# Performance work log

Hardware: AMD Instinct MI355X
Metric: run time of the kernel (lower is better)

The kernel has to match this reference:

```python
import jax, jax.numpy as jnp
import numpy as np

D_MODEL = 1024
D_SAE = 16384
BATCH = 4096
EPS = 1e-8

def _layer_norm(v):
    # v: [B, D]; matches torch branch with keepdim=True
    mean = v.mean(axis=1, keepdims=True)
    var = ((v - mean) ** 2).mean(axis=1, keepdims=True)
    return (v - mean) / jnp.sqrt(var + EPS)

def setup_inputs() -> dict:
    key = jax.random.key(0)
    k1, k2 = jax.random.split(key)
    x = jax.random.normal(k1, (BATCH, 2 * D_MODEL), dtype=jnp.float32)
    # kaiming_uniform on [d_model, d_sae]: bound = sqrt(6 / fan_in), fan_in = d_sae (torch default mode='fan_in' on dim 1)
    bound = float(np.sqrt(6.0 / D_SAE))
    W_enc = jax.random.uniform(k2, (D_MODEL, D_SAE), dtype=jnp.float32, minval=-bound, maxval=bound)
    W_dec = W_enc.T  # init ties decoder to encoder transpose
    b_enc = jnp.zeros((D_SAE,), dtype=jnp.float32)
    b_dec = jnp.zeros((D_MODEL,), dtype=jnp.float32)
    return {"x": x, "W_enc": W_enc, "b_enc": b_enc, "W_dec": W_dec, "b_dec": b_dec, "k": 64}

def reference(x, W_enc, b_enc, W_dec, b_dec, k):
    B = x.shape[0]
    d_model = W_enc.shape[0]
    src = x[:, :d_model]
    tgt = x[:, d_model:]
    # standardize_method == 'layer_norm_and_diff_layer_norm'
    diff = _layer_norm(_layer_norm(tgt) - _layer_norm(src))  # [B, D]
    # encode
    acts = jax.nn.relu(diff @ W_enc + b_enc)  # [B, F]
    # batch top-k on decoder-norm-scaled scores
    dec_norms = jnp.linalg.norm(W_dec, axis=1)  # [F]
    flat_scores = (acts * dec_norms).reshape(-1)  # [B*F]
    _, topk_idx = jax.lax.top_k(flat_scores, k * B)
    mask = jnp.zeros_like(flat_scores).at[topk_idx].set(1.0).reshape(B, -1)
    sparse_acts = acts * mask  # [B, F]
    # decode
    recon = sparse_acts @ W_dec + b_dec  # [B, D]
    return recon
```

## Files before the change

kernel.cpp:

```cpp
#include <hip/hip_runtime.h>
#include <math.h>

#define D_MODEL 1024
#define D_SAE   16384
#define BATCH   4096
#define NTOT    (1ull * BATCH * D_SAE)
#define LN_EPS  1e-8
#define EPS_M   3e-4f
#define ROW_CAP 256
#define CAND_CAP  (4 * 1024 * 1024)
#define CAND2_CAP 65536

using bf16x8 = __attribute__((ext_vector_type(8))) short;
using f32x4  = __attribute__((ext_vector_type(4))) float;

__device__ inline unsigned short f2bf(float f) {
  unsigned u = __float_as_uint(f);
  return (unsigned short)((u + 0x7fffu + ((u >> 16) & 1u)) >> 16);
}
__device__ inline float bf2f(unsigned short h) {
  return __uint_as_float((unsigned)h << 16);
}

__device__ inline double blockReduceSum256(double v, double* lds) {
#pragma unroll
  for (int off = 32; off > 0; off >>= 1) v += __shfl_down(v, off, 64);
  int lane = threadIdx.x & 63, wid = threadIdx.x >> 6;
  __syncthreads();
  if (lane == 0) lds[wid] = v;
  __syncthreads();
  return lds[0] + lds[1] + lds[2] + lds[3];
}
__device__ inline int blockReduceSumInt256(int v, int* lds) {
#pragma unroll
  for (int off = 32; off > 0; off >>= 1) v += __shfl_down(v, off, 64);
  int lane = threadIdx.x & 63, wid = threadIdx.x >> 6;
  __syncthreads();
  if (lane == 0) lds[wid] = v;
  __syncthreads();
  return lds[0] + lds[1] + lds[2] + lds[3];
}

__device__ inline int wave_append(bool pred, int* counter) {
  unsigned long long m = __ballot(pred);
  int lane = threadIdx.x & 63;
  int pos = -1;
  if (m) {
    int ldr = __ffsll((long long)m) - 1;
    int base = 0;
    if (lane == ldr) base = atomicAdd(counter, __popcll(m));
    base = __shfl(base, ldr, 64);
    if (pred) pos = base + __popcll(m & ((1ull << lane) - 1ull));
  }
  return pos;
}

__device__ inline void hist_scan_desc(const int* __restrict__ hist, int nbins, int need,
                                      int& bsel, int& cumsel) {
  int t = threadIdx.x;
  int chunk = nbins >> 6;
  int topbase = nbins - t * chunk;
  int psum = 0;
  for (int i = 1; i <= chunk; ++i) psum += hist[topbase - i];
  int incl = psum;
#pragma unroll
  for (int off = 1; off < 64; off <<= 1) {
    int v = __shfl_up(incl, off, 64);
    if (t >= off) incl += v;
  }
  int excl = incl - psum;
  bool hit = (excl < need) && (excl + psum >= need);
  unsigned long long m = __ballot(hit);
  int tb = m ? (__ffsll((long long)m) - 1) : 63;
  int exb = __shfl(excl, tb, 64);
  int res_b = 0, res_c = 0;
  if (t == tb) {
    int c = exb;
    int b = nbins - tb * chunk - 1;
    int bend = b - chunk;
    for (; b > 0 && b > bend; --b) {
      int cc = hist[b];
      if (c + cc >= need) break;
      c += cc;
    }
    res_b = b; res_c = c;
  }
  bsel = __shfl(res_b, tb, 64);
  cumsel = __shfl(res_c, tb, 64);
}

__device__ inline void ln_row_fp64(const float* __restrict__ row, double* lds, double d[4]) {
  int t = threadIdx.x;
  float4 s4 = *(const float4*)(row + t * 4);
  float4 t4 = *(const float4*)(row + D_MODEL + t * 4);
  double s[4] = {s4.x, s4.y, s4.z, s4.w};
  double tt[4] = {t4.x, t4.y, t4.z, t4.w};
  double ms = blockReduceSum256(s[0] + s[1] + s[2] + s[3], lds) / D_MODEL;
  double mt = blockReduceSum256(tt[0] + tt[1] + tt[2] + tt[3], lds) / D_MODEL;
  double vs = 0, vt = 0;
#pragma unroll
  for (int i = 0; i < 4; i++) { double a = s[i] - ms; vs += a * a; a = tt[i] - mt; vt += a * a; }
  vs = blockReduceSum256(vs, lds) / D_MODEL;
  vt = blockReduceSum256(vt, lds) / D_MODEL;
  double rs = sqrt(vs + LN_EPS), rt = sqrt(vt + LN_EPS);
  double u[4];
#pragma unroll
  for (int i = 0; i < 4; i++) u[i] = (tt[i] - mt) / rt - (s[i] - ms) / rs;
  double mu = blockReduceSum256(u[0] + u[1] + u[2] + u[3], lds) / D_MODEL;
  double vu = 0;
#pragma unroll
  for (int i = 0; i < 4; i++) { double a = u[i] - mu; vu += a * a; }
  vu = blockReduceSum256(vu, lds) / D_MODEL;
  double ru = sqrt(vu + LN_EPS);
#pragma unroll
  for (int i = 0; i < 4; i++) d[i] = (u[i] - mu) / ru;
}

__global__ __launch_bounds__(256) void ln_kernel(const float* __restrict__ x,
                                                 short* __restrict__ Ahi, short* __restrict__ Alo) {
  int wv = threadIdx.x >> 6, lane = threadIdx.x & 63;
  int b = (blockIdx.x << 2) | wv;
  const float* row = x + (size_t)b * (2 * D_MODEL);
  float s[16], t[16];
  const float4* s4p = (const float4*)(row + lane * 16);
  const float4* t4p = (const float4*)(row + D_MODEL + lane * 16);
  double sum_s = 0, sum_t = 0;
#pragma unroll
  for (int q = 0; q < 4; ++q) {
    float4 a = s4p[q], c = t4p[q];
    s[q * 4 + 0] = a.x; s[q * 4 + 1] = a.y; s[q * 4 + 2] = a.z; s[q * 4 + 3] = a.w;
    t[q * 4 + 0] = c.x; t[q * 4 + 1] = c.y; t[q * 4 + 2] = c.z; t[q * 4 + 3] = c.w;
  }
#pragma unroll
  for (int i = 0; i < 16; ++i) { sum_s += s[i]; sum_t += t[i]; }
#pragma unroll
  for (int off = 1; off < 64; off <<= 1) {
    sum_s += __shfl_xor(sum_s, off, 64);
    sum_t += __shfl_xor(sum_t, off, 64);
  }
  double ms = sum_s / D_MODEL, mt_ = sum_t / D_MODEL;
  double vs = 0, vt = 0;
#pragma unroll
  for (int i = 0; i < 16; ++i) {
    double a = s[i] - ms; vs += a * a;
    double c = t[i] - mt_; vt += c * c;
  }
#pragma unroll
  for (int off = 1; off < 64; off <<= 1) {
    vs += __shfl_xor(vs, off, 64);
    vt += __shfl_xor(vt, off, 64);
  }
  double rs = sqrt(vs / D_MODEL + LN_EPS), rt = sqrt(vt / D_MODEL + LN_EPS);
  double u[16], su = 0;
#pragma unroll
  for (int i = 0; i < 16; ++i) { u[i] = (t[i] - mt_) / rt - (s[i] - ms) / rs; su += u[i]; }
#pragma unroll
  for (int off = 1; off < 64; off <<= 1) su += __shfl_xor(su, off, 64);
  double mu = su / D_MODEL, vu = 0;
#pragma unroll
  for (int i = 0; i < 16; ++i) { double a = u[i] - mu; vu += a * a; }
#pragma unroll
  for (int off = 1; off < 64; off <<= 1) vu += __shfl_xor(vu, off, 64);
  double ru = sqrt(vu / D_MODEL + LN_EPS);
  int mtb = b >> 7, ml = b & 127;
#pragma unroll
  for (int blk8 = 0; blk8 < 2; ++blk8) {
    short h8[8], l8[8];
#pragma unroll
    for (int e = 0; e < 8; ++e) {
      int i = blk8 * 8 + e;
      double dd = (u[i] - mu) / ru;
      float f = (float)dd;
      unsigned short hh = f2bf(f);
      h8[e] = (short)hh;
      l8[e] = (short)f2bf(f - bf2f(hh));
    }
    int gi = lane * 16 + blk8 * 8;
    int ks = gi >> 5, kc = (gi >> 3) & 3;
    size_t base = ((((size_t)mtb * 32 + ks) * 4 + kc) * 128 + ml) * 8;
    *(float4*)&Ahi[base] = *(float4*)h8;
    *(float4*)&Alo[base] = *(float4*)l8;
  }
}

__global__ __launch_bounds__(256) void norm_kernel(const float* __restrict__ Wdec,
                                                   double* __restrict__ g64, float* __restrict__ g32) {
  int wv = threadIdx.x >> 6, lane = threadIdx.x & 63;
  int j = (blockIdx.x << 2) | wv;
  const float4* rowp = (const float4*)(Wdec + (size_t)j * D_MODEL);
  double a = 0;
#pragma unroll
  for (int q = 0; q < 4; ++q) {
    float4 w = rowp[lane + q * 64];
    a += (double)w.x * w.x + (double)w.y * w.y + (double)w.z * w.z + (double)w.w * w.w;
  }
#pragma unroll
  for (int off = 32; off > 0; off >>= 1) a += __shfl_down(a, off, 64);
  if (lane == 0) { double g = sqrt(a); g64[j] = g; g32[j] = (float)g; }
}

__global__ __launch_bounds__(256) void wsplit_kernel(const float* __restrict__ Wenc,
                                                     short* __restrict__ Whi, short* __restrict__ Wlo) {
  __shared__ short sh[4096];
  __shared__ short sl[4096];
  int blk = blockIdx.x;
  int nt = blk >> 5, ks = blk & 31;
  int t = threadIdx.x;
  int r = t >> 3;
  int cg = t & 7;
  int kc = r >> 3, e = r & 7;
  const float* src = Wenc + (size_t)(ks * 32 + r) * D_SAE + nt * 128 + cg;
#pragma unroll
  for (int j = 0; j < 16; ++j) {
    float f = src[j * 8];
    unsigned short hh = f2bf(f);
    short ll = (short)f2bf(f - bf2f(hh));
    int c = j * 8 + cg;
    sh[kc * 1024 + c * 8 + e] = (short)hh;
    sl[kc * 1024 + c * 8 + e] = ll;
  }
  __syncthreads();
  size_t obase = ((size_t)nt * 32 + ks) * 4096;
  *(float4*)&Whi[obase + t * 16]     = *(const float4*)&sh[t * 16];
  *(float4*)&Whi[obase + t * 16 + 8] = *(const float4*)&sh[t * 16 + 8];
  *(float4*)&Wlo[obase + t * 16]     = *(const float4*)&sl[t * 16];
  *(float4*)&Wlo[obase + t * 16 + 8] = *(const float4*)&sl[t * 16 + 8];
}

__global__ __launch_bounds__(256) void wdecsplit_kernel(const float* __restrict__ Wdec,
                                                        short* __restrict__ wdech) {
  int j = blockIdx.x, t = threadIdx.x;
  float4 w = *(const float4*)(Wdec + (size_t)j * D_MODEL + t * 4);
  short4 h;
  h.x = (short)f2bf(w.x); h.y = (short)f2bf(w.y);
  h.z = (short)f2bf(w.z); h.w = (short)f2bf(w.w);
  *(short4*)&wdech[(size_t)j * D_MODEL + t * 4] = h;
}

__global__ __launch_bounds__(256) void hist_gemm(
    const short* __restrict__ Whi, const short* __restrict__ Ahi,
    const float* __restrict__ benc, const float* __restrict__ g32,
    int* __restrict__ ghist) {
  __shared__ short sA[4096];
  __shared__ short sB[4096];
  __shared__ int h[4][2048];
  const int tid = threadIdx.x;
  const int lane = tid & 63;
  const int w = tid >> 6;
  const int wm = (w >> 1) * 64, wn = (w & 1) * 64;
  int lin = blockIdx.x;
  int mt = lin >> 7, nt = lin & 127;
  const int col0 = nt * 128;
  for (int i = tid; i < 8192; i += 256) ((int*)h)[i] = 0;
  const size_t atile = (size_t)mt * 131072;
  const size_t btile = (size_t)nt * 131072;
  f32x4 acc[4][4] = {};
  const int kcl = lane >> 4, l15 = lane & 15;

  float4 a0, a1, b0, b1;
  {
    const float4* ah4 = (const float4*)(Ahi + atile);
    const float4* bh4 = (const float4*)(Whi + btile);
    a0 = ah4[tid]; a1 = ah4[tid + 256];
    b0 = bh4[tid]; b1 = bh4[tid + 256];
  }
  for (int ks = 0; ks < 32; ++ks) {
    __syncthreads();
    *(float4*)&sA[(size_t)tid * 8] = a0;
    *(float4*)&sA[(size_t)(tid + 256) * 8] = a1;
    *(float4*)&sB[(size_t)tid * 8] = b0;
    *(float4*)&sB[(size_t)(tid + 256) * 8] = b1;
    __syncthreads();
    if (ks < 31) {
      const float4* ah4 = (const float4*)(Ahi + atile + (ks + 1) * 4096);
      const float4* bh4 = (const float4*)(Whi + btile + (ks + 1) * 4096);
      a0 = ah4[tid]; a1 = ah4[tid + 256];
      b0 = bh4[tid]; b1 = bh4[tid + 256];
    }
    bf16x8 ahf[4];
#pragma unroll
    for (int fm = 0; fm < 4; ++fm)
      ahf[fm] = *(const bf16x8*)&sA[(kcl * 128 + wm + fm * 16 + l15) * 8];
#pragma unroll
    for (int fn = 0; fn < 4; ++fn) {
      bf16x8 bh = *(const bf16x8*)&sB[(kcl * 128 + wn + fn * 16 + l15) * 8];
#pragma unroll
      for (int fm = 0; fm < 4; ++fm)
        acc[fm][fn] = __builtin_amdgcn_mfma_f32_16x16x32_bf16(ahf[fm], bh, acc[fm][fn], 0, 0, 0);
    }
  }
#pragma unroll
  for (int fn = 0; fn < 4; ++fn) {
    int col = col0 + wn + fn * 16 + l15;
    float g = g32[col], be = benc[col];
#pragma unroll
    for (int fm = 0; fm < 4; ++fm) {
#pragma unroll
      for (int r = 0; r < 4; ++r) {
        float z = acc[fm][fn][r] + be;
        float s = z > 0.f ? z * g : 0.f;
        unsigned bits = __float_as_uint(s);
        if (bits) atomicAdd(&h[w][bits >> 21], 1);
      }
    }
  }
  __syncthreads();
  for (int i = tid; i < 2048; i += 256) {
    int v = h[0][i] + h[1][i] + h[2][i] + h[3][i];
    if (v) atomicAdd(&ghist[i], v);
  }
}

__global__ __launch_bounds__(256, 3) void extract_gemm128(
    const short* __restrict__ Whi, const short* __restrict__ Wlo,
    const short* __restrict__ Ahi, const short* __restrict__ Alo,
    const float* __restrict__ benc, const float* __restrict__ g32,
    int* __restrict__ ctrl, int* __restrict__ cand_idx, float* __restrict__ cand_sc,
    int* __restrict__ ghist) {
  __shared__ short sA[8192];
  __shared__ short sB[8192];

  const int tid = threadIdx.x;
  const int lane = tid & 63;
  const int w = tid >> 6;
  const int wm = (w >> 1) * 64, wn = (w & 1) * 64;

  int lin = blockIdx.x;
  int xcd = lin & 7, j = lin >> 3;
  int mt = (xcd << 2) | (j & 3);
  int nt = j >> 2;
  const int row0 = mt * 128, col0 = nt * 128;

  const size_t atile = (size_t)mt * 131072;
  const size_t btile = (size_t)nt * 131072;

  f32x4 acc[4][4] = {};
  const int kcl = lane >> 4, l15 = lane & 15;

  float4 a0, a1, a2, a3, b0, b1, b2, b3;
  {
    const float4* ah4 = (const float4*)(Ahi + atile);
    const float4* al4 = (const float4*)(Alo + atile);
    const float4* bh4 = (const float4*)(Whi + btile);
    const float4* bl4 = (const float4*)(Wlo + btile);
    a0 = ah4[tid]; a1 = ah4[tid + 256];
    a2 = al4[tid]; a3 = al4[tid + 256];
    b0 = bh4[tid]; b1 = bh4[tid + 256];
    b2 = bl4[tid]; b3 = bl4[tid + 256];
  }

  for (int ks = 0; ks < 32; ++ks) {
    __syncthreads();
    *(float4*)&sA[(size_t)tid * 8] = a0;
    *(float4*)&sA[(size_t)(tid + 256) * 8] = a1;
    *(float4*)&sA[(size_t)(512 + tid) * 8] = a2;
    *(float4*)&sA[(size_t)(512 + tid + 256) * 8] = a3;
    *(float4*)&sB[(size_t)tid * 8] = b0;
    *(float4*)&sB[(size_t)(tid + 256) * 8] = b1;
    *(float4*)&sB[(size_t)(512 + tid) * 8] = b2;
    *(float4*)&sB[(size_t)(512 + tid + 256) * 8] = b3;
    __syncthreads();
    if (ks < 31) {
      const int o = (ks + 1) * 4096;
      const float4* ah4 = (const float4*)(Ahi + atile + o);
      const float4* al4 = (const float4*)(Alo + atile + o);
      const float4* bh4 = (const float4*)(Whi + btile + o);
      const float4* bl4 = (const float4*)(Wlo + btile + o);
      a0 = ah4[tid]; a1 = ah4[tid + 256];
      a2 = al4[tid]; a3 = al4[tid + 256];
      b0 = bh4[tid]; b1 = bh4[tid + 256];
      b2 = bl4[tid]; b3 = bl4[tid + 256];
    }
    bf16x8 ahf[4], alf[4];
#pragma unroll
    for (int fm = 0; fm < 4; ++fm) {
      int off = (kcl * 128 + wm + fm * 16 + l15) * 8;
      ahf[fm] = *(const bf16x8*)&sA[off];
      alf[fm] = *(const bf16x8*)&sA[4096 + off];
    }
#pragma unroll
    for (int fn = 0; fn < 4; ++fn) {
      int boff = (kcl * 128 + wn + fn * 16 + l15) * 8;
      bf16x8 bh = *(const bf16x8*)&sB[boff];
      bf16x8 bl = *(const bf16x8*)&sB[4096 + boff];
#pragma unroll
      for (int fm = 0; fm < 4; ++fm) {
        acc[fm][fn] = __builtin_amdgcn_mfma_f32_16x16x32_bf16(ahf[fm], bh, acc[fm][fn], 0, 0, 0);
        acc[fm][fn] = __builtin_amdgcn_mfma_f32_16x16x32_bf16(alf[fm], bh, acc[fm][fn], 0, 0, 0);
        acc[fm][fn] = __builtin_amdgcn_mfma_f32_16x16x32_bf16(ahf[fm], bl, acc[fm][fn], 0, 0, 0);
      }
    }
  }

  int* hh = (int*)sA;
  const int l4r = lane >> 4;
  unsigned thrBits = (unsigned)ctrl[1];
  __syncthreads();
  for (int i = tid; i < 2050; i += 256) hh[i] = 0;
  __syncthreads();
  int cnt = 0;
#pragma unroll
  for (int fn = 0; fn < 4; ++fn) {
    int col = col0 + wn + fn * 16 + l15;
    float g = g32[col], be = benc[col];
#pragma unroll
    for (int fm = 0; fm < 4; ++fm) {
#pragma unroll
      for (int r = 0; r < 4; ++r) {
        float z = acc[fm][fn][r] + be;
        float s = z > 0.f ? z * g : 0.f;
        unsigned bits = __float_as_uint(s);
        if (bits >= thrBits) { cnt++; atomicAdd(&hh[bits >> 21], 1); }
      }
    }
  }
  int my = 0;
  if (cnt) my = atomicAdd(&hh[2048], cnt);
  __syncthreads();
  if (tid == 0) hh[2049] = atomicAdd(&ctrl[2], hh[2048]);
  for (int i = tid; i < 2048; i += 256)
    if (hh[i]) atomicAdd(&ghist[i], hh[i]);
  __syncthreads();
  int pos = hh[2049] + my;
#pragma unroll
  for (int fn = 0; fn < 4; ++fn) {
    int col = col0 + wn + fn * 16 + l15;
    float g = g32[col], be = benc[col];
#pragma unroll
    for (int fm = 0; fm < 4; ++fm) {
      int rowb = row0 + wm + fm * 16 + l4r * 4;
#pragma unroll
      for (int r = 0; r < 4; ++r) {
        float z = acc[fm][fn][r] + be;
        float s = z > 0.f ? z * g : 0.f;
        if (__float_as_uint(s) >= thrBits) {
          if (pos < CAND_CAP) { cand_idx[pos] = (rowb + r) * D_SAE + col; cand_sc[pos] = s; }
          pos++;
        }
      }
    }
  }
}

template <int MODE>
__global__ __launch_bounds__(256) void mfma_gemm(
    const float* __restrict__ Wenc,
    const short* __restrict__ Ahi, const short* __restrict__ Alo,
    const float* __restrict__ benc, const float* __restrict__ g32,
    int* __restrict__ ghist, int* __restrict__ ctrl,
    int* __restrict__ cand_idx, float* __restrict__ cand_sc) {
  __shared__ short sA[8192];
  __shared__ short sB[8192];
  __shared__ int h[(MODE == 0) ? 2048 : 2];
  const int tid = threadIdx.x;
  const int lane = tid & 63;
  const int w = tid >> 6;
  const int wm = (w >> 1) * 64, wn = (w & 1) * 64;
  int lin = blockIdx.x;
  int mt, nt;
  if (MODE == 0) { mt = lin >> 7; nt = lin & 127; }
  else { int xcd = lin & 7, j = lin >> 3; mt = j & 31; nt = (xcd << 4) | (j >> 5); }
  const int row0 = mt * 128, col0 = nt * 128;
  if (MODE == 0) { for (int i = tid; i < 2048; i += 256) h[i] = 0; }
  else if (tid == 0) h[0] = 0;
  const int nl = tid & 127;
  const int half = tid >> 7;
  const float* wbase = Wenc + (size_t)col0 + nl;
  const size_t atile = (size_t)mt * 131072;
  f32x4 acc[4][4] = {};
  const int kcl = lane >> 4, l15 = lane & 15;
  float4 a0, a1, a2, a3;
  float bfv[16];
  {
    const float4* ah4 = (const float4*)(Ahi + atile);
    const float4* al4 = (const float4*)(Alo + atile);
    a0 = ah4[tid]; a1 = ah4[tid + 256];
    a2 = al4[tid]; a3 = al4[tid + 256];
#pragma unroll
    for (int p = 0; p < 4; ++p)
#pragma unroll
      for (int i = 0; i < 4; ++i)
        bfv[p * 4 + i] = wbase[(size_t)(p * 8 + half * 4 + i) * D_SAE];
  }
  for (int ks = 0; ks < 32; ++ks) {
    short hb[16], lb[16];
#pragma unroll
    for (int q = 0; q < 16; ++q) {
      unsigned short hh = f2bf(bfv[q]);
      hb[q] = (short)hh;
      lb[q] = (short)f2bf(bfv[q] - bf2f(hh));
    }
    __syncthreads();
    *(float4*)&sA[(size_t)tid * 8] = a0;
    *(float4*)&sA[(size_t)(tid + 256) * 8] = a1;
    *(float4*)&sA[(size_t)(512 + tid) * 8] = a2;
    *(float4*)&sA[(size_t)(512 + tid + 256) * 8] = a3;
#pragma unroll
    for (int p = 0; p < 4; ++p) {
      int boff = p * 1024 + nl * 8 + half * 4;
      *(short4*)&sB[boff] = make_short4(hb[p * 4], hb[p * 4 + 1], hb[p * 4 + 2], hb[p * 4 + 3]);
      *(short4*)&sB[4096 + boff] = make_short4(lb[p * 4], lb[p * 4 + 1], lb[p * 4 + 2], lb[p * 4 + 3]);
    }
    __syncthreads();
    if (ks < 31) {
      const float4* ah4 = (const float4*)(Ahi + atile + (ks + 1) * 4096);
      const float4* al4 = (const float4*)(Alo + atile + (ks + 1) * 4096);
      a0 = ah4[tid]; a1 = ah4[tid + 256];
      a2 = al4[tid]; a3 = al4[tid + 256];
      const int k0n = (ks + 1) * 32;
#pragma unroll
      for (int p = 0; p < 4; ++p)
#pragma unroll
        for (int i = 0; i < 4; ++i)
          bfv[p * 4 + i] = wbase[(size_t)(k0n + p * 8 + half * 4 + i) * D_SAE];
    }
    bf16x8 ahf[4], alf[4];
#pragma unroll
    for (int fm = 0; fm < 4; ++fm) {
      int off = (kcl * 128 + wm + fm * 16 + l15) * 8;
      ahf[fm] = *(const bf16x8*)&sA[off];
      alf[fm] = *(const bf16x8*)&sA[4096 + off];
    }
#pragma unroll
    for (int fn = 0; fn < 4; ++fn) {
      int boff = (kcl * 128 + wn + fn * 16 + l15) * 8;
      bf16x8 bh = *(const bf16x8*)&sB[boff];
      bf16x8 bl = *(const bf16x8*)&sB[4096 + boff];
#pragma unroll
      for (int fm = 0; fm < 4; ++fm) {
        acc[fm][fn] = __builtin_amdgcn_mfma_f32_16x16x32_bf16(ahf[fm], bh, acc[fm][fn], 0, 0, 0);
        acc[fm][fn] = __builtin_amdgcn_mfma_f32_16x16x32_bf16(alf[fm], bh, acc[fm][fn], 0, 0, 0);
        acc[fm][fn] = __builtin_amdgcn_mfma_f32_16x16x32_bf16(ahf[fm], bl, acc[fm][fn], 0, 0, 0);
      }
    }
  }
  const int l4r = lane >> 4;
  if (MODE == 0) {
#pragma unroll
    for (int fn = 0; fn < 4; ++fn) {
      int col = col0 + wn + fn * 16 + l15;
      float g = g32[col], be = benc[col];
#pragma unroll
      for (int fm = 0; fm < 4; ++fm) {
#pragma unroll
        for (int r = 0; r < 4; ++r) {
          float z = acc[fm][fn][r] + be;
          float s = z > 0.f ? z * g : 0.f;
          unsigned bits = __float_as_uint(s);
          if (bits) atomicAdd(&h[bits >> 21], 1);
        }
      }
    }
    __syncthreads();
    for (int i = tid; i < 2048; i += 256)
      if (h[i]) atomicAdd(&ghist[i], h[i]);
  } else {
    unsigned thrBits = (unsigned)ctrl[1];
    int cnt = 0;
#pragma unroll
    for (int fn = 0; fn < 4; ++fn) {
      int col = col0 + wn + fn * 16 + l15;
      float g = g32[col], be = benc[col];
#pragma unroll
      for (int fm = 0; fm < 4; ++fm) {
#pragma unroll
        for (int r = 0; r < 4; ++r) {
          float z = acc[fm][fn][r] + be;
          float s = z > 0.f ? z * g : 0.f;
          cnt += (__float_as_uint(s) >= thrBits) ? 1 : 0;
        }
      }
    }
    int my = 0;
    if (cnt) my = atomicAdd(&h[0], cnt);
    __syncthreads();
    if (tid == 0) h[1] = atomicAdd(&ctrl[2], h[0]);
    __syncthreads();
    int pos = h[1] + my;
#pragma unroll
    for (int fn = 0; fn < 4; ++fn) {
      int col = col0 + wn + fn * 16 + l15;
      float g = g32[col], be = benc[col];
#pragma unroll
      for (int fm = 0; fm < 4; ++fm) {
        int rowb = row0 + wm + fm * 16 + l4r * 4;
#pragma unroll
        for (int r = 0; r < 4; ++r) {
          float z = acc[fm][fn][r] + be;
          float s = z > 0.f ? z * g : 0.f;
          if (__float_as_uint(s) >= thrBits) {
            if (pos < CAND_CAP) { cand_idx[pos] = (rowb + r) * D_SAE + col; cand_sc[pos] = s; }
            pos++;
          }
        }
      }
    }
  }
}

__global__ void find_coarse_kernel(const int* __restrict__ gh, int* ctrl,
                                   const int* __restrict__ kptr, int sub) {
  long long kB = (long long)kptr[0] * BATCH;
  long long needl = (kB + 500000 + sub - 1) / sub;
  long long fl = 720000 / sub;
  if (needl < fl) needl = fl;
  int b, cum;
  hist_scan_desc(gh, 2048, (int)needl, b, cum);
  if (threadIdx.x == 0) {
    long long est_incl = (long long)sub * (cum + gh[b]);
    if (est_incl > 3500000LL && (long long)sub * cum >= kB + 120000LL) b = b + 1;
    ctrl[1] = (int)(((unsigned)b) << 21);
  }
}

__global__ __launch_bounds__(256) void chist_kernel(const float* __restrict__ cand_sc,
                                                    const int* __restrict__ ctrl,
                                                    int* __restrict__ ghist, int pass) {
  __shared__ int h[2048];
  int nb = (pass == 2) ? 1024 : 2048;
  for (int i = threadIdx.x; i < nb; i += 256) h[i] = 0;
  __syncthreads();
  int n = ctrl[2]; if (n > CAND_CAP) n = CAND_CAP;
  unsigned sel1 = 0, sel22 = 0;
  if (pass == 1) sel1 = (unsigned)ctrl[3];
  if (pass == 2) sel22 = ((unsigned)ctrl[3] << 11) | (unsigned)ctrl[5];
  for (int i = blockIdx.x * 256 + threadIdx.x; i < n; i += gridDim.x * 256) {
    unsigned bits = __float_as_uint(cand_sc[i]);
    if (pass == 0) atomicAdd(&h[bits >> 21], 1);
    else if (pass == 1) { if ((bits >> 21) == sel1) atomicAdd(&h[(bits >> 10) & 0x7FFu], 1); }
    else { if ((bits >> 10) == sel22) atomicAdd(&h[bits & 0x3FFu], 1); }
  }
  __syncthreads();
  for (int i = threadIdx.x; i < nb; i += 256)
    if (h[i]) atomicAdd(&ghist[i], h[i]);
}

__global__ void cfind_kernel(const int* __restrict__ hist, int* ctrl,
                             const int* __restrict__ kptr, int pass) {
  int kB = kptr[0] * BATCH;
  int need, nbins;
  if (pass == 0)      { need = kB;                       nbins = 2048; }
  else if (pass == 1) { need = kB - ctrl[4];             nbins = 2048; }
  else                { need = kB - ctrl[4] - ctrl[6];   nbins = 1024; }
  int b, cum;
  hist_scan_desc(hist, nbins, need, b, cum);
  if (threadIdx.x == 0) {
    if (pass == 0)      { ctrl[3] = b; ctrl[4] = cum; }
    else if (pass == 1) { ctrl[5] = b; ctrl[6] = cum; }
    else {
      unsigned vbits = ((unsigned)ctrl[3] << 21) | ((unsigned)ctrl[5] << 10) | (unsigned)b;
      float V = __uint_as_float(vbits);
      float* cf = (float*)ctrl;
      cf[8] = V; cf[9] = V + EPS_M; cf[10] = V - EPS_M;
    }
  }
}

__global__ __launch_bounds__(256) void band_kernel(const int* __restrict__ cand_idx,
    const float* __restrict__ cand_sc, const float* __restrict__ g32,
    int* ctrl, int* row_cnt, int* row_feat, float* row_act, int* cand2_idx) {
  const float* cf = (const float*)ctrl;
  float hi = cf[9], lo = cf[10];
  int n = ctrl[2]; if (n > CAND_CAP) n = CAND_CAP;
  int lane = threadIdx.x & 63;
  int defc = 0;
  for (int i = blockIdx.x * 256 + threadIdx.x; i < n; i += gridDim.x * 256) {
    float s = cand_sc[i];
    int flat = cand_idx[i];
    if (s > hi) {
      int b = flat >> 14, j = flat & (D_SAE - 1);
      int p = atomicAdd(&row_cnt[b], 1);
      if (p < ROW_CAP) { row_feat[b * ROW_CAP + p] = j; row_act[b * ROW_CAP + p] = s / g32[j]; }
      defc++;
    }
    bool isc = (s <= hi) && (s >= lo);
    int pos = wave_append(isc, &ctrl[12]);
    if (isc && pos >= 0 && pos < CAND2_CAP) cand2_idx[pos] = flat;
  }
#pragma unroll
  for (int off = 32; off > 0; off >>= 1) defc += __shfl_down(defc, off, 64);
  if (lane == 0 && defc) atomicAdd(&ctrl[11], defc);
}

__global__ __launch_bounds__(256) void cand2_score_kernel(const int* __restrict__ ctrl,
    const int* __restrict__ cand2_idx, const float* __restrict__ x,
    const float* __restrict__ Wdec, const float* __restrict__ benc,
    const double* __restrict__ g64, double* __restrict__ cand2_sc) {
  __shared__ double lds[4];
  int n2 = ctrl[12]; if (n2 > CAND2_CAP) n2 = CAND2_CAP;
  int t = threadIdx.x;
  for (int c = blockIdx.x; c < n2; c += gridDim.x) {
    int flat = cand2_idx[c];
    int b = flat >> 14, j = flat & (D_SAE - 1);
    double d[4];
    ln_row_fp64(x + (size_t)b * (2 * D_MODEL), lds, d);
    float4 w4 = *(const float4*)(Wdec + (size_t)j * D_MODEL + t * 4);
    double a = d[0] * (double)w4.x + d[1] * (double)w4.y + d[2] * (double)w4.z + d[3] * (double)w4.w;
    double z = blockReduceSum256(a, lds) + (double)benc[j];
    double sc = z > 0 ? z * g64[j] : 0.0;
    if (t == 0) cand2_sc[c] = sc;
  }
}

__global__ __launch_bounds__(256) void cand2_rank_kernel(const int* __restrict__ ctrl,
    const int* __restrict__ cand2_idx, const double* __restrict__ cand2_sc,
    const double* __restrict__ g64, const int* __restrict__ kptr,
    int* row_cnt, int* row_feat, float* row_act) {
  __shared__ int lds[4];
  int n2 = ctrl[12]; if (n2 > CAND2_CAP) n2 = CAND2_CAP;
  int kB = kptr[0] * BATCH;
  int fill = kB - ctrl[11];
  int t = threadIdx.x;
  for (int c = blockIdx.x; c < n2; c += gridDim.x) {
    double sc = cand2_sc[c];
    int fc = cand2_idx[c];
    int cnt = 0;
    for (int y = t; y < n2; y += 256) {
      double sy = cand2_sc[y];
      if (sy > sc || (sy == sc && cand2_idx[y] < fc)) cnt++;
    }
    cnt = blockReduceSumInt256(cnt, lds);
    if (t == 0 && cnt < fill) {
      int b = fc >> 14, j = fc & (D_SAE - 1);
      int p = atomicAdd(&row_cnt[b], 1);
      if (p < ROW_CAP) { row_feat[b * ROW_CAP + p] = j; row_act[b * ROW_CAP + p] = (float)(sc / g64[j]); }
    }
  }
}

__global__ __launch_bounds__(256) void recon_bf16_kernel(const int* __restrict__ row_cnt,
    const int* __restrict__ row_feat, const float* __restrict__ row_act,
    const short* __restrict__ wdech, const float* __restrict__ bdec, float* __restrict__ out) {
  int b = blockIdx.x, t = threadIdx.x;
  float4 acc0 = *(const float4*)&bdec[t * 4];
  float4 acc1 = make_float4(0.f, 0.f, 0.f, 0.f);
  int n = row_cnt[b]; if (n > ROW_CAP) n = ROW_CAP;
  const int* rf = row_feat + (size_t)b * ROW_CAP;
  const float* ra = row_act + (size_t)b * ROW_CAP;
  int p = 0;
  for (; p + 2 <= n; p += 2) {
    int j0 = rf[p], j1 = rf[p + 1];
    float v0 = ra[p], v1 = ra[p + 1];
    short4 h0 = *(const short4*)&wdech[(size_t)j0 * D_MODEL + t * 4];
    short4 h1 = *(const short4*)&wdech[(size_t)j1 * D_MODEL + t * 4];
    acc0.x += v0 * bf2f((unsigned short)h0.x); acc0.y += v0 * bf2f((unsigned short)h0.y);
    acc0.z += v0 * bf2f((unsigned short)h0.z); acc0.w += v0 * bf2f((unsigned short)h0.w);
    acc1.x += v1 * bf2f((unsigned short)h1.x); acc1.y += v1 * bf2f((unsigned short)h1.y);
    acc1.z += v1 * bf2f((unsigned short)h1.z); acc1.w += v1 * bf2f((unsigned short)h1.w);
  }
  if (p < n) {
    int j0 = rf[p]; float v0 = ra[p];
    short4 h0 = *(const short4*)&wdech[(size_t)j0 * D_MODEL + t * 4];
    acc0.x += v0 * bf2f((unsigned short)h0.x); acc0.y += v0 * bf2f((unsigned short)h0.y);
    acc0.z += v0 * bf2f((unsigned short)h0.z); acc0.w += v0 * bf2f((unsigned short)h0.w);
  }
  acc0.x += acc1.x; acc0.y += acc1.y; acc0.z += acc1.z; acc0.w += acc1.w;
  *(float4*)(out + (size_t)b * D_MODEL + t * 4) = acc0;
}

__global__ __launch_bounds__(256) void recon_kernel(const int* __restrict__ row_cnt,
    const int* __restrict__ row_feat, const float* __restrict__ row_act,
    const float* __restrict__ Wdec, const float* __restrict__ bdec, float* __restrict__ out) {
  int b = blockIdx.x, t = threadIdx.x;
  float4 acc0 = *(const float4*)&bdec[t * 4];
  float4 acc1 = make_float4(0.f, 0.f, 0.f, 0.f);
  int n = row_cnt[b]; if (n > ROW_CAP) n = ROW_CAP;
  const int* rf = row_feat + (size_t)b * ROW_CAP;
  const float* ra = row_act + (size_t)b * ROW_CAP;
  int p = 0;
  for (; p + 2 <= n; p += 2) {
    int j0 = rf[p], j1 = rf[p + 1];
    float v0 = ra[p], v1 = ra[p + 1];
    float4 w0 = *(const float4*)(Wdec + (size_t)j0 * D_MODEL + t * 4);
    float4 w1 = *(const float4*)(Wdec + (size_t)j1 * D_MODEL + t * 4);
    acc0.x += v0 * w0.x; acc0.y += v0 * w0.y; acc0.z += v0 * w0.z; acc0.w += v0 * w0.w;
    acc1.x += v1 * w1.x; acc1.y += v1 * w1.y; acc1.z += v1 * w1.z; acc1.w += v1 * w1.w;
  }
  if (p < n) {
    int j0 = rf[p]; float v0 = ra[p];
    float4 w0 = *(const float4*)(Wdec + (size_t)j0 * D_MODEL + t * 4);
    acc0.x += v0 * w0.x; acc0.y += v0 * w0.y; acc0.z += v0 * w0.z; acc0.w += v0 * w0.w;
  }
  acc0.x += acc1.x; acc0.y += acc1.y; acc0.z += acc1.z; acc0.w += acc1.w;
  *(float4*)(out + (size_t)b * D_MODEL + t * 4) = acc0;
}

extern "C" void kernel_launch(void* const* d_in, const int* in_sizes, int n_in,
                              void* d_out, int out_size, void* d_ws, size_t ws_size,
                              hipStream_t stream) {
  const float* x    = (const float*)d_in[0];
  const float* Wenc = (const float*)d_in[1];
  const float* benc = (const float*)d_in[2];
  const float* Wdec = (const float*)d_in[3];
  const float* bdec = (const float*)d_in[4];
  const int*   kptr = (const int*)d_in[5];
  float* out = (float*)d_out;

  char* ws = (char*)d_ws;
  size_t off = 0;
  short*  Ahi       = (short*)(ws + off);  off += (size_t)BATCH * D_MODEL * 2;
  short*  Alo       = (short*)(ws + off);  off += (size_t)BATCH * D_MODEL * 2;
  int*    cand_idx  = (int*)(ws + off);    off += (size_t)CAND_CAP * 4;
  float*  cand_sc   = (float*)(ws + off);  off += (size_t)CAND_CAP * 4;
  int*    row_feat  = (int*)(ws + off);    off += (size_t)BATCH * ROW_CAP * 4;
  float*  row_act   = (float*)(ws + off);  off += (size_t)BATCH * ROW_CAP * 4;
  int*    cand2_idx = (int*)(ws + off);    off += (size_t)CAND2_CAP * 4;
  double* cand2_sc  = (double*)(ws + off); off += (size_t)CAND2_CAP * 8;
  double* g64       = (double*)(ws + off); off += (size_t)D_SAE * 8;
  float*  g32       = (float*)(ws + off);  off += (size_t)D_SAE * 4;
  char*   zbase     = ws + off;
  int* ghist   = (int*)(zbase);
  int* h1      = (int*)(zbase + 8192);
  int* h2      = (int*)(zbase + 16384);
  int* h3      = (int*)(zbase + 24576);
  int* ctrl    = (int*)(zbase + 28672);
  int* row_cnt = (int*)(zbase + 28928);
  size_t zbytes = 28928 + (size_t)BATCH * 4;
  size_t small_need = off + zbytes;
  if (small_need > ws_size) return;

  size_t big_off = (small_need + 255) & ~(size_t)255;
  short* Whi = (short*)(ws + big_off);
  short* Wlo = Whi + (size_t)D_MODEL * D_SAE;
  size_t big_need = big_off + (size_t)D_MODEL * D_SAE * 4;
  const bool big = (big_need <= ws_size);

  short* wdech = (short*)cand_idx;

  hipMemsetAsync(zbase, 0, zbytes, stream);

  ln_kernel<<<BATCH / 4, 256, 0, stream>>>(x, Ahi, Alo);
  norm_kernel<<<D_SAE / 4, 256, 0, stream>>>(Wdec, g64, g32);
  if (big) {
    wsplit_kernel<<<4096, 256, 0, stream>>>(Wenc, Whi, Wlo);
    hist_gemm<<<256, 256, 0, stream>>>(Whi, Ahi, benc, g32, ghist);
    find_coarse_kernel<<<1, 64, 0, stream>>>(ghist, ctrl, kptr, 16);
    extract_gemm128<<<4096, 256, 0, stream>>>(Whi, Wlo, Ahi, Alo, benc, g32, ctrl, cand_idx, cand_sc, h1);
  } else {
    mfma_gemm<0><<<256, 256, 0, stream>>>(Wenc, Ahi, Alo, benc, g32, ghist, ctrl, nullptr, nullptr);
    find_coarse_kernel<<<1, 64, 0, stream>>>(ghist, ctrl, kptr, 16);
    mfma_gemm<1><<<4096, 256, 0, stream>>>(Wenc, Ahi, Alo, benc, g32, nullptr, ctrl, cand_idx, cand_sc);
    chist_kernel<<<1024, 256, 0, stream>>>(cand_sc, ctrl, h1, 0);
  }
  cfind_kernel<<<1, 64, 0, stream>>>(h1, ctrl, kptr, 0);
  chist_kernel<<<1024, 256, 0, stream>>>(cand_sc, ctrl, h2, 1);
  cfind_kernel<<<1, 64, 0, stream>>>(h2, ctrl, kptr, 1);
  chist_kernel<<<1024, 256, 0, stream>>>(cand_sc, ctrl, h3, 2);
  cfind_kernel<<<1, 64, 0, stream>>>(h3, ctrl, kptr, 2);
  band_kernel<<<1024, 256, 0, stream>>>(cand_idx, cand_sc, g32, ctrl, row_cnt, row_feat, row_act, cand2_idx);
  cand2_score_kernel<<<4096, 256, 0, stream>>>(ctrl, cand2_idx, x, Wdec, benc, g64, cand2_sc);
  cand2_rank_kernel<<<2048, 256, 0, stream>>>(ctrl, cand2_idx, cand2_sc, g64, kptr, row_cnt, row_feat, row_act);
  if (big) {
    wdecsplit_kernel<<<D_SAE, 256, 0, stream>>>(Wdec, wdech);
    recon_bf16_kernel<<<BATCH, 256, 0, stream>>>(row_cnt, row_feat, row_act, wdech, bdec, out);
  } else {
    recon_kernel<<<BATCH, 256, 0, stream>>>(row_cnt, row_feat, row_act, Wdec, bdec, out);
  }
}
```

Measured before the change: 683.7 us.

## Double-buffer B tile in LDS and load A fragments directly from global

The extract GEMM kernel stops staging the activation (A) tile through shared memory. Each wave now reads its bf16 hi/lo A fragments straight from the pre-tiled global layout. The weight (B) tile is double-buffered in LDS, so each k-step needs one barrier instead of two and the next tile is written while the current one is consumed. This trades LDS traffic and barriers for redundant global/L2 reads of A across the two column-waves, and uses more registers for the held B fragments.

After: 676.0 us. About the same (-1.1%).

```diff
diff --git a/kernel.cpp b/kernel.cpp
--- a/kernel.cpp
+++ b/kernel.cpp
@@ -317,8 +317,7 @@
     const float* __restrict__ benc, const float* __restrict__ g32,
     int* __restrict__ ctrl, int* __restrict__ cand_idx, float* __restrict__ cand_sc,
     int* __restrict__ ghist) {
-  __shared__ short sA[8192];
-  __shared__ short sB[8192];
+  __shared__ short sB[2][8192];
 
   const int tid = threadIdx.x;
   const int lane = tid & 63;
@@ -337,65 +336,69 @@
   f32x4 acc[4][4] = {};
   const int kcl = lane >> 4, l15 = lane & 15;
 
-  float4 a0, a1, a2, a3, b0, b1, b2, b3;
+  float4 b0, b1, b2, b3;
   {
-    const float4* ah4 = (const float4*)(Ahi + atile);
-    const float4* al4 = (const float4*)(Alo + atile);
     const float4* bh4 = (const float4*)(Whi + btile);
     const float4* bl4 = (const float4*)(Wlo + btile);
-    a0 = ah4[tid]; a1 = ah4[tid + 256];
-    a2 = al4[tid]; a3 = al4[tid + 256];
     b0 = bh4[tid]; b1 = bh4[tid + 256];
     b2 = bl4[tid]; b3 = bl4[tid + 256];
   }
+  *(float4*)&sB[0][(size_t)tid * 8] = b0;
+  *(float4*)&sB[0][(size_t)(tid + 256) * 8] = b1;
+  *(float4*)&sB[0][(size_t)(512 + tid) * 8] = b2;
+  *(float4*)&sB[0][(size_t)(512 + tid + 256) * 8] = b3;
+  __syncthreads();
+  int cur = 0;
+
+  const int afrag = kcl * 1024 + (wm + l15) * 8;
 
   for (int ks = 0; ks < 32; ++ks) {
-    __syncthreads();
-    *(float4*)&sA[(size_t)tid * 8] = a0;
-    *(float4*)&sA[(size_t)(tid + 256) * 8] = a1;
-    *(float4*)&sA[(size_t)(512 + tid) * 8] = a2;
-    *(float4*)&sA[(size_t)(512 + tid + 256) * 8] = a3;
-    *(float4*)&sB[(size_t)tid * 8] = b0;
-    *(float4*)&sB[(size_t)(tid + 256) * 8] = b1;
-    *(float4*)&sB[(size_t)(512 + tid) * 8] = b2;
-    *(float4*)&sB[(size_t)(512 + tid + 256) * 8] = b3;
-    __syncthreads();
     if (ks < 31) {
       const int o = (ks + 1) * 4096;
-      const float4* ah4 = (const float4*)(Ahi + atile + o);
-      const float4* al4 = (const float4*)(Alo + atile + o);
       const float4* bh4 = (const float4*)(Whi + btile + o);
       const float4* bl4 = (const float4*)(Wlo + btile + o);
-      a0 = ah4[tid]; a1 = ah4[tid + 256];
-      a2 = al4[tid]; a3 = al4[tid + 256];
       b0 = bh4[tid]; b1 = bh4[tid + 256];
       b2 = bl4[tid]; b3 = bl4[tid + 256];
     }
+    const short* ah = Ahi + atile + (size_t)ks * 4096 + afrag;
+    const short* al = Alo + atile + (size_t)ks * 4096 + afrag;
     bf16x8 ahf[4], alf[4];
 #pragma unroll
     for (int fm = 0; fm < 4; ++fm) {
-      int off = (kcl * 128 + wm + fm * 16 + l15) * 8;
-      ahf[fm] = *(const bf16x8*)&sA[off];
-      alf[fm] = *(const bf16x8*)&sA[4096 + off];
-    }
+      ahf[fm] = *(const bf16x8*)&ah[fm * 128];
+      alf[fm] = *(const bf16x8*)&al[fm * 128];
+    }
+    const short* tB = sB[cur];
+    bf16x8 bh[4], bl[4];
 #pragma unroll
     for (int fn = 0; fn < 4; ++fn) {
       int boff = (kcl * 128 + wn + fn * 16 + l15) * 8;
-      bf16x8 bh = *(const bf16x8*)&sB[boff];
-      bf16x8 bl = *(const bf16x8*)&sB[4096 + boff];
+      bh[fn] = *(const bf16x8*)&tB[boff];
+      bl[fn] = *(const bf16x8*)&tB[4096 + boff];
+    }
+#pragma unroll
+    for (int fn = 0; fn < 4; ++fn) {
 #pragma unroll
       for (int fm = 0; fm < 4; ++fm) {
-        acc[fm][fn] = __builtin_amdgcn_mfma_f32_16x16x32_bf16(ahf[fm], bh, acc[fm][fn], 0, 0, 0);
-        acc[fm][fn] = __builtin_amdgcn_mfma_f32_16x16x32_bf16(alf[fm], bh, acc[fm][fn], 0, 0, 0);
-        acc[fm][fn] = __builtin_amdgcn_mfma_f32_16x16x32_bf16(ahf[fm], bl, acc[fm][fn], 0, 0, 0);
+        acc[fm][fn] = __builtin_amdgcn_mfma_f32_16x16x32_bf16(ahf[fm], bh[fn], acc[fm][fn], 0, 0, 0);
+        acc[fm][fn] = __builtin_amdgcn_mfma_f32_16x16x32_bf16(alf[fm], bh[fn], acc[fm][fn], 0, 0, 0);
+        acc[fm][fn] = __builtin_amdgcn_mfma_f32_16x16x32_bf16(ahf[fm], bl[fn], acc[fm][fn], 0, 0, 0);
       }
     }
-  }
-
-  int* hh = (int*)sA;
+    if (ks < 31) {
+      short* nB = sB[cur ^ 1];
+      *(float4*)&nB[(size_t)tid * 8] = b0;
+      *(float4*)&nB[(size_t)(tid + 256) * 8] = b1;
+      *(float4*)&nB[(size_t)(512 + tid) * 8] = b2;
+      *(float4*)&nB[(size_t)(512 + tid + 256) * 8] = b3;
+    }
+    __syncthreads();
+    cur ^= 1;
+  }
+
+  int* hh = (int*)sB;
   const int l4r = lane >> 4;
   unsigned thrBits = (unsigned)ctrl[1];
-  __syncthreads();
   for (int i = tid; i < 2050; i += 256) hh[i] = 0;
   __syncthreads();
   int cnt = 0;
```
